# Kernel optimization log

Hardware: AMD Instinct MI355X
Metric: run time of the kernel (lower is better)

## Reference

```python
import jax, jax.numpy as jnp
import numpy as np

N, IN_DIM, HID, B, C = 131072, 256, 256, 8, 128


def setup_inputs() -> dict:
    key = jax.random.key(0)
    ks = jax.random.split(key, 7)
    s_in, s_h = 1.0 / np.sqrt(IN_DIM), 1.0 / np.sqrt(HID)
    return {
        "x": jax.random.normal(ks[0], (N, IN_DIM), dtype=jnp.float32),
        "W_base": jax.random.normal(ks[1], (IN_DIM, HID), dtype=jnp.float32) * s_in,
        "b_base": jax.random.normal(ks[2], (HID,), dtype=jnp.float32) * 0.01,
        "W_clf": jax.random.normal(ks[3], (B, HID, C), dtype=jnp.float32) * s_h,
        "b_clf": jax.random.normal(ks[4], (B, C), dtype=jnp.float32) * 0.01,
        "W_est": jax.random.normal(ks[5], (B, HID), dtype=jnp.float32) * s_h,
        "b_est": jax.random.normal(ks[6], (B,), dtype=jnp.float32) * 0.01,
    }


def reference(x, W_base, b_base, W_clf, b_clf, W_est, b_est):
    # base trunk: [N, HID]
    base_out = x @ W_base + b_base
    # per-branch estimated loss: [N, B]  (each branch's estimate_loss -> (N,1), viewed as (N,))
    est = base_out @ W_est.T + b_est
    # top-1 routing: per-sample argmin over branches (detached in original)
    branch_ids = jnp.argmin(est, axis=1)  # [N] int
    # all-branch logits [N, B, C]; selecting row branch_ids[n] reproduces the
    # per-branch gather -> forward -> scatter of the original exactly
    logits = jnp.einsum("nh,bhc->nbc", base_out, W_clf) + b_clf
    out = jnp.take_along_axis(logits, branch_ids[:, None, None], axis=1)[:, 0, :]  # [N, C]
    return out
```

## Files before the change

### kernel.cpp

```cpp
#include <hip/hip_runtime.h>


#define NROWS 131072
#define ROWS  64
#define XST   260

typedef __bf16 bf16x8 __attribute__((ext_vector_type(8)));
typedef float  f32x4  __attribute__((ext_vector_type(4)));
typedef unsigned short u16x8 __attribute__((ext_vector_type(8)));

__device__ __forceinline__ unsigned short f2bf(float f) {
    unsigned u = __builtin_bit_cast(unsigned, f);
    u += 0x7fffu + ((u >> 16) & 1u);
    return (unsigned short)(u >> 16);
}

__global__ __launch_bounds__(256) void k_prep(const float* __restrict__ Wb,
                                              const float* __restrict__ bb,
                                              const float* __restrict__ Wc,
                                              const float* __restrict__ bc,
                                              const float* __restrict__ We,
                                              const float* __restrict__ be,
                                              double* __restrict__ Wcomb,
                                              double* __restrict__ bcomb,
                                              unsigned short* __restrict__ Wfold,
                                              float* __restrict__ bfold) {
    __shared__ float clf[32][128];
    __shared__ float wbt[32][16];
    __shared__ double red[256];
    __shared__ float part[256];
    int blk = blockIdx.x, tid = threadIdx.x;

    if (blk < 8) {
        int b = blk, k = tid;
        const float4* wbr = (const float4*)(Wb + k * 256);
        const float4* wer = (const float4*)(We + b * 256);
        double a0 = 0.0, a1 = 0.0, a2 = 0.0, a3 = 0.0;
#pragma unroll 8
        for (int j = 0; j < 64; ++j) {
            float4 u = wbr[j], w = wer[j];
            a0 += (double)u.x * (double)w.x;
            a1 += (double)u.y * (double)w.y;
            a2 += (double)u.z * (double)w.z;
            a3 += (double)u.w * (double)w.w;
        }
        Wcomb[b * 256 + k] = (a0 + a1) + (a2 + a3);

        red[k] = (double)bb[k] * (double)We[b * 256 + k];
        __syncthreads();
        for (int s = 128; s; s >>= 1) {
            if (k < s) red[k] += red[k + s];
            __syncthreads();
        }
        if (k == 0) bcomb[b] = red[0] + (double)be[b];
        return;
    }

    if (blk < 16) {
        int b = blk - 8;
        int c = tid & 127, hg = tid >> 7;
        float a = 0.f;
#pragma unroll 16
        for (int h = 0; h < 128; ++h)
            a += bb[hg * 128 + h] * Wc[((b * 256 + hg * 128 + h)) * 128 + c];
        part[tid] = a;
        __syncthreads();
        if (tid < 128) bfold[b * 128 + tid] = part[tid] + part[tid + 128] + bc[b * 128 + tid];
        return;
    }

    int idx0 = blk - 16;
    int kg = idx0 & 15, b = idx0 >> 4;
    int c = tid & 127, kh = tid >> 7;

    float acc[8];
#pragma unroll
    for (int j = 0; j < 8; ++j) acc[j] = 0.f;

    for (int ht = 0; ht < 8; ++ht) {
#pragma unroll
        for (int j = 0; j < 16; ++j) {
            int idx = tid + j * 256;
            int hh = idx >> 7, cc = idx & 127;
            clf[hh][cc] = Wc[(b * 256 + ht * 32 + hh) * 128 + cc];
        }
#pragma unroll
        for (int j = 0; j < 2; ++j) {
            int idx = tid + j * 256;
            int hh = idx & 31, kk = idx >> 5;
            wbt[hh][kk] = Wb[(kg * 16 + kk) * 256 + ht * 32 + hh];
        }
        __syncthreads();
        for (int h = 0; h < 32; ++h) {
            float wc = clf[h][c];
            float4 w0 = *(const float4*)&wbt[h][kh * 8];
            float4 w1 = *(const float4*)&wbt[h][kh * 8 + 4];
            acc[0] += w0.x * wc; acc[1] += w0.y * wc;
            acc[2] += w0.z * wc; acc[3] += w0.w * wc;
            acc[4] += w1.x * wc; acc[5] += w1.y * wc;
            acc[6] += w1.z * wc; acc[7] += w1.w * wc;
        }
        __syncthreads();
    }
    unsigned short o8[8];
#pragma unroll
    for (int j = 0; j < 8; ++j) o8[j] = f2bf(acc[j]);
    u16x8 pk;
#pragma unroll
    for (int j = 0; j < 8; ++j) pk[j] = o8[j];
    int base = (b * 128 + c) * 256 + kg * 16 + kh * 8;
    *(u16x8*)&Wfold[base] = pk;
}

__global__ __launch_bounds__(256, 2) void k_main(const float* __restrict__ x,
                                                 const double* __restrict__ Wcomb,
                                                 const double* __restrict__ bcomb,
                                                 const unsigned short* __restrict__ Wfold,
                                                 const float* __restrict__ bfold,
                                                 float* __restrict__ out) {
    __shared__ float xs[ROWS * XST];
    __shared__ unsigned char list[8][ROWS];
    __shared__ int cnt[8];
    __shared__ unsigned char tasks[16];
    __shared__ int ntasks;

    const int tid = threadIdx.x;
    const int blk = blockIdx.x;
    const int wave = tid >> 6, lane = tid & 63;
    const int bl = lane & 7, kc = lane >> 3;
    const size_t rowbase = (size_t)blk * ROWS;

    if (tid < 8) cnt[tid] = 0;

    double w0[8], w1[8], w2[8], w3[8];
    {
        const double* wb = Wcomb + bl * 256 + kc * 4;
#pragma unroll
        for (int t = 0; t < 8; ++t) {
            double2 p0 = *(const double2*)(wb + t * 32);
            double2 p1 = *(const double2*)(wb + t * 32 + 2);
            w0[t] = p0.x; w1[t] = p0.y; w2[t] = p1.x; w3[t] = p1.y;
        }
    }
    const double bco = bcomb[bl];

#pragma unroll 4
    for (int it = 0; it < 16; ++it) {
        int idx = it * 256 + tid;
        int r = idx >> 6, gq = idx & 63;
        float4 v = *(const float4*)(x + (rowbase + r) * 256 + gq * 4);
        *(float4*)&xs[r * XST + gq * 4] = v;
    }
    __syncthreads();

    for (int rr = 0; rr < 16; ++rr) {
        int r = wave * 16 + rr;
        const float* xr = xs + r * XST + kc * 4;
        double a0 = 0.0, a1 = 0.0, a2 = 0.0, a3 = 0.0;
#pragma unroll
        for (int t = 0; t < 8; ++t) {
            float4 v = *(const float4*)(xr + t * 32);
            a0 += (double)v.x * w0[t];
            a1 += (double)v.y * w1[t];
            a2 += (double)v.z * w2[t];
            a3 += (double)v.w * w3[t];
        }
        double e = (a0 + a2) + (a1 + a3);
        e += __shfl_xor(e, 8);
        e += __shfl_xor(e, 16);
        e += __shfl_xor(e, 32);
        e += bco;
        int bid = bl;
#pragma unroll
        for (int d = 4; d; d >>= 1) {
            double o = __shfl_xor(e, d);
            int ob = __shfl_xor(bid, d);
            if (o < e || (o == e && ob < bid)) { e = o; bid = ob; }
        }
        if (lane == 0) {
            int p = atomicAdd(&cnt[bid], 1);
            list[bid][p] = (unsigned char)r;
        }
    }
    __syncthreads();

    if (tid == 0) {
        int nt = 0;
#pragma unroll
        for (int b = 0; b < 8; ++b) {
            int ng = (cnt[b] + 15) >> 4;
            for (int g = 0; g < ng; ++g) tasks[nt++] = (unsigned char)((b << 4) | g);
        }
        ntasks = nt;
    }
    __syncthreads();

    const int n16 = lane & 15, quad = lane >> 4;
    const int nt = ntasks;
    for (int t = wave; t < nt; t += 4) {
        int b = tasks[t] >> 4, g = tasks[t] & 15;
        int nb = cnt[b];
        int slot = g * 16 + n16;
        int arid = list[b][slot < nb ? slot : nb - 1];
        const float* ap = xs + arid * XST + quad * 8;

        bf16x8 Af[8];
#pragma unroll
        for (int kt = 0; kt < 8; ++kt) {
            float4 f0 = *(const float4*)(ap + kt * 32);
            float4 f1 = *(const float4*)(ap + kt * 32 + 4);
            u16x8 pk;
            pk[0] = f2bf(f0.x); pk[1] = f2bf(f0.y); pk[2] = f2bf(f0.z); pk[3] = f2bf(f0.w);
            pk[4] = f2bf(f1.x); pk[5] = f2bf(f1.y); pk[6] = f2bf(f1.z); pk[7] = f2bf(f1.w);
            Af[kt] = __builtin_bit_cast(bf16x8, pk);
        }

        const unsigned short* wb = Wfold + (size_t)(b * 128 + n16) * 256 + quad * 8;
        f32x4 acc[8];
#pragma unroll
        for (int ct = 0; ct < 8; ++ct) {
            float bias = bfold[b * 128 + ct * 16 + n16];
            acc[ct] = (f32x4){bias, bias, bias, bias};
        }
#pragma unroll
        for (int kt = 0; kt < 8; ++kt) {
            const unsigned short* wk = wb + kt * 32;
#pragma unroll
            for (int ct = 0; ct < 8; ++ct) {
                bf16x8 Bf = __builtin_bit_cast(bf16x8, *(const u16x8*)(wk + ct * 16 * 256));
                acc[ct] = __builtin_amdgcn_mfma_f32_16x16x32_bf16(Af[kt], Bf, acc[ct], 0, 0, 0);
            }
        }

        int srow[4];
#pragma unroll
        for (int reg = 0; reg < 4; ++reg) {
            int r16 = g * 16 + quad * 4 + reg;
            srow[reg] = r16 < nb ? (int)list[b][r16] : -1;
        }
#pragma unroll
        for (int ct = 0; ct < 8; ++ct) {
#pragma unroll
            for (int reg = 0; reg < 4; ++reg)
                if (srow[reg] >= 0)
                    out[(rowbase + srow[reg]) * 128 + ct * 16 + n16] = acc[ct][reg];
        }
    }
}

extern "C" void kernel_launch(void* const* d_in, const int* in_sizes, int n_in,
                              void* d_out, int out_size, void* d_ws, size_t ws_size,
                              hipStream_t stream) {
    const float* x  = (const float*)d_in[0];
    const float* Wb = (const float*)d_in[1];
    const float* bb = (const float*)d_in[2];
    const float* Wc = (const float*)d_in[3];
    const float* bc = (const float*)d_in[4];
    const float* We = (const float*)d_in[5];
    const float* be = (const float*)d_in[6];
    float* out = (float*)d_out;

    unsigned char* ws = (unsigned char*)d_ws;
    double* Wcomb = (double*)ws;
    double* bcomb = (double*)(ws + 16384);
    unsigned short* Wfold = (unsigned short*)(ws + 16448);
    float* bfold = (float*)(ws + 540736);

    hipLaunchKernelGGL(k_prep, dim3(144), dim3(256), 0, stream,
                       Wb, bb, Wc, bc, We, be, Wcomb, bcomb, Wfold, bfold);
    hipLaunchKernelGGL(k_main, dim3(NROWS / ROWS), dim3(256), 0, stream,
                       x, Wcomb, bcomb, Wfold, bfold, out);
}
```

Before: 369.9 us.

## Replace per-branch row grouping with dense all-branch MFMA and masked stores

Drops the shared-memory routing lists, atomics and task scheduling. Each block now computes logits for all 8 branches over 32 rows with MFMA and stores only the entries whose argmin branch matches. Block size shrinks to 32 rows and occupancy rises to 4 blocks per SM. This removes serialization and the load imbalance of the gather, but does roughly 8x the classifier FLOPs and re-reads more weight data.

New measurement: 679.2 us. +83.6%, slower.

```diff
diff --git a/kernel.cpp b/kernel.cpp
--- a/kernel.cpp
+++ b/kernel.cpp
@@ -2,7 +2,7 @@
 
 
 #define NROWS 131072
-#define ROWS  64
+#define ROWS  32
 #define XST   260
 
 typedef __bf16 bf16x8 __attribute__((ext_vector_type(8)));
@@ -112,25 +112,19 @@
     *(u16x8*)&Wfold[base] = pk;
 }
 
-__global__ __launch_bounds__(256, 2) void k_main(const float* __restrict__ x,
+__global__ __launch_bounds__(256, 4) void k_main(const float* __restrict__ x,
                                                  const double* __restrict__ Wcomb,
                                                  const double* __restrict__ bcomb,
                                                  const unsigned short* __restrict__ Wfold,
                                                  const float* __restrict__ bfold,
                                                  float* __restrict__ out) {
     __shared__ float xs[ROWS * XST];
-    __shared__ unsigned char list[8][ROWS];
-    __shared__ int cnt[8];
-    __shared__ unsigned char tasks[16];
-    __shared__ int ntasks;
+    __shared__ int bids[ROWS];
 
     const int tid = threadIdx.x;
-    const int blk = blockIdx.x;
     const int wave = tid >> 6, lane = tid & 63;
     const int bl = lane & 7, kc = lane >> 3;
-    const size_t rowbase = (size_t)blk * ROWS;
-
-    if (tid < 8) cnt[tid] = 0;
+    const size_t rowbase = (size_t)blockIdx.x * ROWS;
 
     double w0[8], w1[8], w2[8], w3[8];
     {
@@ -144,8 +138,8 @@
     }
     const double bco = bcomb[bl];
 
-#pragma unroll 4
-    for (int it = 0; it < 16; ++it) {
+#pragma unroll
+    for (int it = 0; it < 8; ++it) {
         int idx = it * 256 + tid;
         int r = idx >> 6, gq = idx & 63;
         float4 v = *(const float4*)(x + (rowbase + r) * 256 + gq * 4);
@@ -153,8 +147,8 @@
     }
     __syncthreads();
 
-    for (int rr = 0; rr < 16; ++rr) {
-        int r = wave * 16 + rr;
+    for (int rr = 0; rr < 8; ++rr) {
+        int r = wave * 8 + rr;
         const float* xr = xs + r * XST + kc * 4;
         double a0 = 0.0, a1 = 0.0, a2 = 0.0, a3 = 0.0;
 #pragma unroll
@@ -177,73 +171,49 @@
             int ob = __shfl_xor(bid, d);
             if (o < e || (o == e && ob < bid)) { e = o; bid = ob; }
         }
-        if (lane == 0) {
-            int p = atomicAdd(&cnt[bid], 1);
-            list[bid][p] = (unsigned char)r;
-        }
+        if (lane == 0) bids[r] = bid;
     }
     __syncthreads();
 
-    if (tid == 0) {
-        int nt = 0;
-#pragma unroll
-        for (int b = 0; b < 8; ++b) {
-            int ng = (cnt[b] + 15) >> 4;
-            for (int g = 0; g < ng; ++g) tasks[nt++] = (unsigned char)((b << 4) | g);
-        }
-        ntasks = nt;
-    }
-    __syncthreads();
-
+    const int rg = wave & 1, chalf = wave >> 1;
     const int n16 = lane & 15, quad = lane >> 4;
-    const int nt = ntasks;
-    for (int t = wave; t < nt; t += 4) {
-        int b = tasks[t] >> 4, g = tasks[t] & 15;
-        int nb = cnt[b];
-        int slot = g * 16 + n16;
-        int arid = list[b][slot < nb ? slot : nb - 1];
-        const float* ap = xs + arid * XST + quad * 8;
-
-        bf16x8 Af[8];
-#pragma unroll
-        for (int kt = 0; kt < 8; ++kt) {
-            float4 f0 = *(const float4*)(ap + kt * 32);
-            float4 f1 = *(const float4*)(ap + kt * 32 + 4);
-            u16x8 pk;
-            pk[0] = f2bf(f0.x); pk[1] = f2bf(f0.y); pk[2] = f2bf(f0.z); pk[3] = f2bf(f0.w);
-            pk[4] = f2bf(f1.x); pk[5] = f2bf(f1.y); pk[6] = f2bf(f1.z); pk[7] = f2bf(f1.w);
-            Af[kt] = __builtin_bit_cast(bf16x8, pk);
-        }
-
-        const unsigned short* wb = Wfold + (size_t)(b * 128 + n16) * 256 + quad * 8;
-        f32x4 acc[8];
-#pragma unroll
-        for (int ct = 0; ct < 8; ++ct) {
+
+    const float* ap = xs + (rg * 16 + n16) * XST + quad * 8;
+    bf16x8 Af[8];
+#pragma unroll
+    for (int kt = 0; kt < 8; ++kt) {
+        float4 f0 = *(const float4*)(ap + kt * 32);
+        float4 f1 = *(const float4*)(ap + kt * 32 + 4);
+        u16x8 pk;
+        pk[0] = f2bf(f0.x); pk[1] = f2bf(f0.y); pk[2] = f2bf(f0.z); pk[3] = f2bf(f0.w);
+        pk[4] = f2bf(f1.x); pk[5] = f2bf(f1.y); pk[6] = f2bf(f1.z); pk[7] = f2bf(f1.w);
+        Af[kt] = __builtin_bit_cast(bf16x8, pk);
+    }
+
+    int mybid[4];
+#pragma unroll
+    for (int reg = 0; reg < 4; ++reg)
+        mybid[reg] = bids[rg * 16 + quad * 4 + reg];
+
+    for (int b = 0; b < 8; ++b) {
+#pragma unroll 2
+        for (int c4 = 0; c4 < 4; ++c4) {
+            int ct = chalf * 4 + c4;
+            const unsigned short* wp =
+                Wfold + (size_t)(b * 128 + ct * 16 + n16) * 256 + quad * 8;
+            bf16x8 Bf[8];
+#pragma unroll
+            for (int kt = 0; kt < 8; ++kt)
+                Bf[kt] = __builtin_bit_cast(bf16x8, *(const u16x8*)(wp + kt * 32));
             float bias = bfold[b * 128 + ct * 16 + n16];
-            acc[ct] = (f32x4){bias, bias, bias, bias};
-        }
-#pragma unroll
-        for (int kt = 0; kt < 8; ++kt) {
-            const unsigned short* wk = wb + kt * 32;
-#pragma unroll
-            for (int ct = 0; ct < 8; ++ct) {
-                bf16x8 Bf = __builtin_bit_cast(bf16x8, *(const u16x8*)(wk + ct * 16 * 256));
-                acc[ct] = __builtin_amdgcn_mfma_f32_16x16x32_bf16(Af[kt], Bf, acc[ct], 0, 0, 0);
-            }
-        }
-
-        int srow[4];
-#pragma unroll
-        for (int reg = 0; reg < 4; ++reg) {
-            int r16 = g * 16 + quad * 4 + reg;
-            srow[reg] = r16 < nb ? (int)list[b][r16] : -1;
-        }
-#pragma unroll
-        for (int ct = 0; ct < 8; ++ct) {
+            f32x4 acc = {bias, bias, bias, bias};
+#pragma unroll
+            for (int kt = 0; kt < 8; ++kt)
+                acc = __builtin_amdgcn_mfma_f32_16x16x32_bf16(Af[kt], Bf[kt], acc, 0, 0, 0);
 #pragma unroll
             for (int reg = 0; reg < 4; ++reg)
-                if (srow[reg] >= 0)
-                    out[(rowbase + srow[reg]) * 128 + ct * 16 + n16] = acc[ct][reg];
+                if (mybid[reg] == b)
+                    out[(rowbase + rg * 16 + quad * 4 + reg) * 128 + ct * 16 + n16] = acc[reg];
         }
     }
 }
```
